# Performance work log

Hardware: AMD Instinct MI355X
Metric: run time of the kernel (lower is better)

Reference implementation:

```python
import jax, jax.numpy as jnp
import numpy as np

DMODEL = 1024
N_MAMBAS = 4
D_INNER = 2 * DMODEL          # expand = 2
D_STATE = 16                  # mamba_ssm default
D_CONV = 4                    # mamba_ssm default
DT_RANK = DMODEL // 16        # ceil(d_model/16) = 64


def setup_inputs() -> dict:
    key = jax.random.key(0)
    ks = jax.random.split(key, 8)
    B, L, n = 2, 4096, N_MAMBAS
    f32 = jnp.float32
    x = jax.random.normal(ks[0], (B, L, DMODEL), f32)
    in_w = jax.random.normal(ks[1], (n, 2 * D_INNER, DMODEL), f32) * 0.02
    conv_w = jax.random.normal(ks[2], (n, D_INNER, D_CONV), f32) * 0.1
    conv_b = jnp.zeros((n, D_INNER), f32)
    xproj_w = jax.random.normal(ks[3], (n, DT_RANK + 2 * D_STATE, D_INNER), f32) * 0.02
    dt_w = jax.random.normal(ks[4], (n, D_INNER, DT_RANK), f32) * 0.02
    # softplus-inverse of dt_init ~ 0.01 (mamba-style dt bias init)
    dt_b = jnp.log(jnp.expm1(jnp.full((n, D_INNER), 0.01, f32)))
    # S4D-real init: A_log = log(1..d_state)
    A_log = jnp.log(jnp.broadcast_to(jnp.arange(1, D_STATE + 1, dtype=f32), (n, D_INNER, D_STATE)))
    D_skip = jnp.ones((n, D_INNER), f32)
    out_w = jax.random.normal(ks[5], (n, DMODEL, D_INNER), f32) * 0.02
    return dict(x=x, in_w=in_w, conv_w=conv_w, conv_b=conv_b, xproj_w=xproj_w,
                dt_w=dt_w, dt_b=dt_b, A_log=A_log, D_skip=D_skip, out_w=out_w)


def _mamba(x, in_w, conv_w, conv_b, xproj_w, dt_w, dt_b, A_log, D_skip, out_w):
    # x: (B, Lc, D)
    Bb = x.shape[0]
    xz = jnp.einsum('bld,ed->ble', x, in_w)                 # (B, Lc, 2*D_INNER)
    xi, z = jnp.split(xz, 2, axis=-1)
    # causal depthwise conv over time
    xc = jnp.transpose(xi, (0, 2, 1))                       # (B, D_INNER, Lc)
    xc = jax.lax.conv_general_dilated(xc, conv_w[:, None, :], (1,),
                                      [(D_CONV - 1, 0)], feature_group_count=D_INNER)
    xi = jax.nn.silu(jnp.transpose(xc + conv_b[None, :, None], (0, 2, 1)))  # (B, Lc, D_INNER)
    proj = jnp.einsum('bld,ed->ble', xi, xproj_w)           # (B, Lc, DT_RANK + 2*D_STATE)
    dt = proj[..., :DT_RANK]
    Bm = proj[..., DT_RANK:DT_RANK + D_STATE]
    Cm = proj[..., DT_RANK + D_STATE:]
    dt = jax.nn.softplus(jnp.einsum('blr,dr->bld', dt, dt_w) + dt_b)  # (B, Lc, D_INNER)
    A = -jnp.exp(A_log)                                     # (D_INNER, D_STATE)

    def step(h, inp):
        dt_t, B_t, C_t, x_t = inp                           # (B,Di),(B,Ds),(B,Ds),(B,Di)
        dA = jnp.exp(dt_t[:, :, None] * A)                  # (B, Di, Ds)
        h = dA * h + dt_t[:, :, None] * B_t[:, None, :] * x_t[:, :, None]
        return h, jnp.einsum('bds,bs->bd', h, C_t)

    h0 = jnp.zeros((Bb, D_INNER, D_STATE), x.dtype)
    xs_t = (jnp.swapaxes(dt, 0, 1), jnp.swapaxes(Bm, 0, 1),
            jnp.swapaxes(Cm, 0, 1), jnp.swapaxes(xi, 0, 1))
    _, ys = jax.lax.scan(step, h0, xs_t)                    # (Lc, B, D_INNER)
    y = jnp.swapaxes(ys, 0, 1) + xi * D_skip                # (B, Lc, D_INNER)
    y = y * jax.nn.silu(z)
    return jnp.einsum('ble,de->bld', y, out_w)              # (B, Lc, D)


def reference(x, in_w, conv_w, conv_b, xproj_w, dt_w, dt_b, A_log, D_skip, out_w):
    B, L, D = x.shape
    n = N_MAMBAS
    # strided slices x[:, i::n] == reshape(B, L//n, n, D)[:, :, i]
    xs = jnp.transpose(x.reshape(B, L // n, n, D), (2, 0, 1, 3))   # (n, B, Lc, D)
    ys = jax.vmap(_mamba)(xs, in_w, conv_w, conv_b, xproj_w,
                          dt_w, dt_b, A_log, D_skip, out_w)        # (n, B, Lc, D)
    # torch.cat(dim=1) concatenates per-mamba outputs block-wise along seq
    return jnp.transpose(ys, (1, 0, 2, 3)).reshape(B, L, D)
```

## Files before the change

### kernel.cpp

```cpp
#include <hip/hip_runtime.h>
#include <math.h>

#define DM   1024
#define DI   2048
#define DSn  16
#define DTR  64
#define PW   96
#define LS   1024
#define NCH  16
#define CL   64
#define XKS  8

typedef unsigned short u16;
typedef unsigned int   u32;
typedef __attribute__((ext_vector_type(8))) short bf16x8;
typedef __attribute__((ext_vector_type(8))) unsigned short u16x8;
typedef __attribute__((ext_vector_type(4))) float f32x4;

__device__ __forceinline__ void split2(float f, u16& hi, u16& lo) {
  union { float f; unsigned int u; } v; v.f = f;
  hi = (u16)(v.u >> 16);
  union { unsigned int u; float f; } w; w.u = v.u & 0xffff0000u;
  union { float f; unsigned int u; } r; r.f = f - w.f;
  lo = (u16)(r.u >> 16);
}

template<int ROWS>
__device__ __forceinline__ bf16x8 frag(const u16* T, int l4, int row) {
  return *(const bf16x8*)&T[(l4 * ROWS + row) * 8];
}

template<int ROWS>
__device__ __forceinline__ void stage16f(const float* a, u16* Th, u16* Tl, int ra, int half) {
  #pragma unroll
  for (int q = 0; q < 2; ++q) {
    u16x8 vh, vl;
    #pragma unroll
    for (int c = 0; c < 8; ++c) {
      u16 h_, l_;
      split2(a[q * 8 + c], h_, l_);
      vh[c] = h_; vl[c] = l_;
    }
    const int slot = ((half * 2 + q) * ROWS + ra) * 8;
    *(u16x8*)&Th[slot] = vh;
    *(u16x8*)&Tl[slot] = vl;
  }
}

template<int ROWS>
__device__ __forceinline__ void stage8f(const float* a, u16* Th, u16* Tl, int rb, int kq) {
  u16x8 vh, vl;
  #pragma unroll
  for (int c = 0; c < 8; ++c) {
    u16 h_, l_;
    split2(a[c], h_, l_);
    vh[c] = h_; vl[c] = l_;
  }
  const int slot = (kq * ROWS + rb) * 8;
  *(u16x8*)&Th[slot] = vh;
  *(u16x8*)&Tl[slot] = vl;
}

__global__ __launch_bounds__(256) void k_split_x(
    const float* __restrict__ x, u16* __restrict__ xh, u16* __restrict__ xl, int ib0)
{
  const int idx = blockIdx.x * 256 + threadIdx.x;
  const int t = idx >> 8, kq = (idx & 255) * 4;
  const int gt = ib0 * 1024 + t;
  const int j = gt & (LS - 1), ib = gt >> 10;
  const int i = ib >> 1, bb = ib & 1;
  const float4 v = *(const float4*)&x[(size_t)(bb * 4096 + j * 4 + i) * DM + kq];
  ushort4 vh, vl;
  split2(v.x, vh.x, vl.x); split2(v.y, vh.y, vl.y);
  split2(v.z, vh.z, vl.z); split2(v.w, vh.w, vl.w);
  *(ushort4*)&xh[(size_t)t * DM + kq] = vh;
  *(ushort4*)&xl[(size_t)t * DM + kq] = vl;
}

#define KGP 2064
__global__ __launch_bounds__(512, 2) void k_inproj(
    const u16* __restrict__ xh, const u16* __restrict__ xl,
    const float* __restrict__ inwf,
    float* __restrict__ xz, int ib0, int swz)
{
  __shared__ __align__(16) u16 L[2][4][4][KGP];
  const int tid = threadIdx.x;
  int mblk, nblk;
  if (swz) {
    const int o = blockIdx.x;
    const int xcd = o & 7, within = o >> 3;
    mblk = xcd * 4 + (within & 3);
    nblk = within >> 2;
  } else {
    mblk = blockIdx.x; nblk = blockIdx.y;
  }
  const int m0 = mblk << 8, n0 = nblk << 8;
  const int ib = ib0 + (m0 >> 10);
  const int il = (ib >> 1) - (ib0 >> 1);
  const int ra = tid >> 1, half = tid & 1;
  const u16* Aph = xh + (size_t)(m0 + ra) * DM + half * 16;
  const u16* Apl = xl + (size_t)(m0 + ra) * DM + half * 16;
  const float* Bpf = inwf + ((size_t)il * 4096 + n0 + ra) * DM + half * 16;
  const int w = tid >> 6, lane = tid & 63;
  const int wr = w >> 2, wc = w & 3;
  const int l15 = lane & 15, l4 = lane >> 4;

  f32x4 acc[8][4];
  #pragma unroll
  for (int a_ = 0; a_ < 8; ++a_)
    #pragma unroll
    for (int b_ = 0; b_ < 4; ++b_) acc[a_][b_] = (f32x4)(0.f);

  u16x8 ah2[2], al2[2];
  float br[16];

  auto LOADG = [&](int kt) {
    const int k0 = kt * 32;
    ah2[0] = *(const u16x8*)(Aph + k0);
    ah2[1] = *(const u16x8*)(Aph + k0 + 8);
    al2[0] = *(const u16x8*)(Apl + k0);
    al2[1] = *(const u16x8*)(Apl + k0 + 8);
    *(f32x4*)&br[0]  = *(const f32x4*)(Bpf + k0);
    *(f32x4*)&br[4]  = *(const f32x4*)(Bpf + k0 + 4);
    *(f32x4*)&br[8]  = *(const f32x4*)(Bpf + k0 + 8);
    *(f32x4*)&br[12] = *(const f32x4*)(Bpf + k0 + 12);
  };
  auto STORE = [&](int b) {
    #pragma unroll
    for (int q = 0; q < 2; ++q) {
      const int kg = half * 2 + q;
      *(u16x8*)&L[b][0][kg][ra * 8] = ah2[q];
      *(u16x8*)&L[b][1][kg][ra * 8] = al2[q];
      u16x8 vh, vl;
      #pragma unroll
      for (int c = 0; c < 8; ++c) {
        u16 h_, l_;
        split2(br[q * 8 + c], h_, l_);
        vh[c] = h_; vl[c] = l_;
      }
      *(u16x8*)&L[b][2][kg][ra * 8] = vh;
      *(u16x8*)&L[b][3][kg][ra * 8] = vl;
    }
  };
  auto COMPUTE = [&](int b) {
    bf16x8 bh[4], bl[4];
    #pragma unroll
    for (int nf = 0; nf < 4; ++nf) {
      const int col = wc * 64 + nf * 16 + l15;
      bh[nf] = *(const bf16x8*)&L[b][2][l4][col * 8];
      bl[nf] = *(const bf16x8*)&L[b][3][l4][col * 8];
    }
    #pragma unroll
    for (int mf = 0; mf < 8; ++mf) {
      const int row = wr * 128 + mf * 16 + l15;
      bf16x8 ah = *(const bf16x8*)&L[b][0][l4][row * 8];
      bf16x8 al = *(const bf16x8*)&L[b][1][l4][row * 8];
      #pragma unroll
      for (int nf = 0; nf < 4; ++nf) {
        acc[mf][nf] = __builtin_amdgcn_mfma_f32_16x16x32_bf16(ah, bh[nf], acc[mf][nf], 0, 0, 0);
        acc[mf][nf] = __builtin_amdgcn_mfma_f32_16x16x32_bf16(ah, bl[nf], acc[mf][nf], 0, 0, 0);
        acc[mf][nf] = __builtin_amdgcn_mfma_f32_16x16x32_bf16(al, bh[nf], acc[mf][nf], 0, 0, 0);
      }
    }
  };

  const int nk = DM / 32;
  LOADG(0);
  STORE(0);
  if (nk > 1) LOADG(1);
  __syncthreads();
  for (int kt = 0; kt < nk; ++kt) {
    const int c = kt & 1;
    if (kt + 1 < nk) STORE(c ^ 1);
    if (kt + 2 < nk) LOADG(kt + 2);
    COMPUTE(c);
    __syncthreads();
  }

  #pragma unroll
  for (int mf = 0; mf < 8; ++mf) {
    const int row = m0 + wr * 128 + mf * 16 + l4 * 4;
    #pragma unroll
    for (int nf = 0; nf < 4; ++nf) {
      const int col = n0 + wc * 64 + nf * 16 + l15;
      #pragma unroll
      for (int r = 0; r < 4; ++r)
        xz[(size_t)(row + r) * (2 * DI) + col] = acc[mf][nf][r];
    }
  }
}

__global__ __launch_bounds__(256) void k_conv(
    const float* __restrict__ xz, const float* __restrict__ convw,
    const float* __restrict__ convb, float* __restrict__ xib,
    int ib0, int ntok)
{
  const int idx = blockIdx.x * 256 + threadIdx.x;
  if (idx >= ntok * (DI / 4)) return;
  const int t = idx / (DI / 4);
  const int c = (idx - t * (DI / 4)) * 4;
  const int j = t & (LS - 1);
  const int i = (ib0 + (t >> 10)) >> 1;
  float4 acc = *(const float4*)&convb[(size_t)i * DI + c];
  float4 wt[4];
  #pragma unroll
  for (int q = 0; q < 4; ++q)
    wt[q] = *(const float4*)&convw[((size_t)i * DI + c + q) * 4];
  #pragma unroll
  for (int k = 0; k < 4; ++k) {
    const int j2 = j + k - 3;
    if (j2 >= 0) {
      const float4 v = *(const float4*)&xz[(size_t)(t + k - 3) * (2 * DI) + c];
      acc.x = fmaf(v.x, ((const float*)&wt[0])[k], acc.x);
      acc.y = fmaf(v.y, ((const float*)&wt[1])[k], acc.y);
      acc.z = fmaf(v.z, ((const float*)&wt[2])[k], acc.z);
      acc.w = fmaf(v.w, ((const float*)&wt[3])[k], acc.w);
    }
  }
  float4 o;
  o.x = acc.x / (1.f + __expf(-acc.x));
  o.y = acc.y / (1.f + __expf(-acc.y));
  o.z = acc.z / (1.f + __expf(-acc.z));
  o.w = acc.w / (1.f + __expf(-acc.w));
  *(float4*)&xib[(size_t)t * DI + c] = o;
}

__global__ __launch_bounds__(256) void k_xproj_part(
    const float* __restrict__ xif, const float* __restrict__ xwf,
    float* __restrict__ Pp, int ib0, int ntok)
{
  __shared__ __align__(16) u16 Ah[4*64*8], Al[4*64*8];
  __shared__ __align__(16) u16 Bh[4*96*8], Bl[4*96*8];
  const int tid = threadIdx.x;
  const int m0 = blockIdx.x << 6;
  const int ks = blockIdx.y;
  const int kbase = ks * (DI / XKS);
  const int ib = ib0 + (m0 >> 10);
  const int il = (ib >> 1) - (ib0 >> 1);
  const int ra = tid >> 1, half = tid & 1;
  const bool hasA = (tid < 128);
  const bool hasB = (tid < 192);
  const float* Apf = xif + (size_t)(m0 + ra) * DI + kbase + half * 16;
  const float* Bpf = xwf + ((size_t)il * PW + ra) * DI + kbase + half * 16;
  const int w = tid >> 6, lane = tid & 63;
  const int l15 = lane & 15, l4 = lane >> 4;

  f32x4 acc[6];
  #pragma unroll
  for (int b_ = 0; b_ < 6; ++b_) acc[b_] = (f32x4)(0.f);

  float ar[16], br[16];
  if (hasA) {
    #pragma unroll
    for (int q = 0; q < 4; ++q) *(f32x4*)&ar[q*4] = *(const f32x4*)(Apf + q*4);
  }
  if (hasB) {
    #pragma unroll
    for (int q = 0; q < 4; ++q) *(f32x4*)&br[q*4] = *(const f32x4*)(Bpf + q*4);
  }
  const int nk = (DI / XKS) / 32;
  for (int kt = 0; kt < nk; ++kt) {
    __syncthreads();
    if (hasA) stage16f<64>(ar, Ah, Al, ra, half);
    if (hasB) stage16f<96>(br, Bh, Bl, ra, half);
    __syncthreads();
    if (kt + 1 < nk) {
      const int k0 = (kt + 1) * 32;
      if (hasA) {
        #pragma unroll
        for (int q = 0; q < 4; ++q) *(f32x4*)&ar[q*4] = *(const f32x4*)(Apf + k0 + q*4);
      }
      if (hasB) {
        #pragma unroll
        for (int q = 0; q < 4; ++q) *(f32x4*)&br[q*4] = *(const f32x4*)(Bpf + k0 + q*4);
      }
    }
    const int arow = w * 16 + l15;
    bf16x8 ah = frag<64>(Ah, l4, arow);
    bf16x8 al = frag<64>(Al, l4, arow);
    #pragma unroll
    for (int nf = 0; nf < 6; ++nf) {
      const int col = nf * 16 + l15;
      bf16x8 bh = frag<96>(Bh, l4, col);
      bf16x8 bl = frag<96>(Bl, l4, col);
      acc[nf] = __builtin_amdgcn_mfma_f32_16x16x32_bf16(ah, bh, acc[nf], 0, 0, 0);
      acc[nf] = __builtin_amdgcn_mfma_f32_16x16x32_bf16(ah, bl, acc[nf], 0, 0, 0);
      acc[nf] = __builtin_amdgcn_mfma_f32_16x16x32_bf16(al, bh, acc[nf], 0, 0, 0);
    }
  }
  float* outp = Pp + (size_t)ks * ntok * PW;
  const int row = m0 + w * 16 + l4 * 4;
  #pragma unroll
  for (int nf = 0; nf < 6; ++nf) {
    const int col = nf * 16 + l15;
    #pragma unroll
    for (int r = 0; r < 4; ++r)
      outp[(size_t)(row + r) * PW + col] = acc[nf][r];
  }
}

__global__ __launch_bounds__(256) void k_xproj_red(
    const float* __restrict__ Pp, float* __restrict__ projb, int ntok)
{
  const int idx = blockIdx.x * 256 + threadIdx.x;
  if (idx >= ntok * PW) return;
  const size_t plane = (size_t)ntok * PW;
  float s = 0.f;
  #pragma unroll
  for (int ks = 0; ks < XKS; ++ks) s += Pp[(size_t)ks * plane + idx];
  projb[idx] = s;
}

__global__ __launch_bounds__(256) void k_dtproj(
    const float* __restrict__ proj, const float* __restrict__ dtw,
    const float* __restrict__ dtbias, float* __restrict__ dtout,
    int dstride, int ib0)
{
  __shared__ float As[16][132];
  __shared__ float Bs[16][132];
  const int tid = threadIdx.x;
  const int n0 = blockIdx.x << 7;
  const int m0 = blockIdx.y << 7;
  const int ib = ib0 + (m0 >> 10);
  const int i  = ib >> 1;
  const int ar = tid >> 2, kq = tid & 3;
  const float* A0 = proj + (size_t)(m0 + ar) * PW + kq * 4;
  const float* A1 = A0 + (size_t)64 * PW;
  const float* Wb = dtw + (size_t)i * DI * DTR;
  const float* B0 = Wb + (size_t)(n0 + ar) * DTR + kq * 4;
  const float* B1 = B0 + (size_t)64 * DTR;
  const int tx = tid & 15, ty = tid >> 4;
  float acc[8][8] = {};
  for (int kt = 0; kt < DTR / 16; ++kt) {
    const int k0 = kt * 16;
    float4 a0 = *(const float4*)(A0 + k0);
    float4 a1 = *(const float4*)(A1 + k0);
    float4 b0 = *(const float4*)(B0 + k0);
    float4 b1 = *(const float4*)(B1 + k0);
    __syncthreads();
    As[kq*4+0][ar] = a0.x; As[kq*4+1][ar] = a0.y; As[kq*4+2][ar] = a0.z; As[kq*4+3][ar] = a0.w;
    As[kq*4+0][ar+64] = a1.x; As[kq*4+1][ar+64] = a1.y; As[kq*4+2][ar+64] = a1.z; As[kq*4+3][ar+64] = a1.w;
    Bs[kq*4+0][ar] = b0.x; Bs[kq*4+1][ar] = b0.y; Bs[kq*4+2][ar] = b0.z; Bs[kq*4+3][ar] = b0.w;
    Bs[kq*4+0][ar+64] = b1.x; Bs[kq*4+1][ar+64] = b1.y; Bs[kq*4+2][ar+64] = b1.z; Bs[kq*4+3][ar+64] = b1.w;
    __syncthreads();
    #pragma unroll
    for (int k = 0; k < 16; ++k) {
      const float4 av0 = *(const float4*)&As[k][ty*8];
      const float4 av1 = *(const float4*)&As[k][ty*8+4];
      const float4 bv0 = *(const float4*)&Bs[k][tx*8];
      const float4 bv1 = *(const float4*)&Bs[k][tx*8+4];
      const float aa[8] = {av0.x,av0.y,av0.z,av0.w,av1.x,av1.y,av1.z,av1.w};
      const float bv[8] = {bv0.x,bv0.y,bv0.z,bv0.w,bv1.x,bv1.y,bv1.z,bv1.w};
      #pragma unroll
      for (int r = 0; r < 8; ++r)
        #pragma unroll
        for (int c = 0; c < 8; ++c)
          acc[r][c] = fmaf(aa[r], bv[c], acc[r][c]);
    }
  }
  float bias[8];
  #pragma unroll
  for (int c = 0; c < 8; ++c) bias[c] = dtbias[(size_t)i * DI + n0 + tx*8 + c];
  #pragma unroll
  for (int r = 0; r < 8; ++r) {
    const int t = m0 + ty*8 + r;
    #pragma unroll
    for (int c = 0; c < 8; ++c) {
      float u = acc[r][c] + bias[c];
      float sp = (u > 20.f) ? u : log1pf(__expf(u));
      dtout[(size_t)t * dstride + n0 + tx*8 + c] = sp;
    }
  }
}

__global__ __launch_bounds__(256) void k_scan_part(
    const float* __restrict__ projb, const float* dtp, int dstride,
    const float* __restrict__ xib, const float* __restrict__ A_log,
    float* __restrict__ Pbuf, float* __restrict__ Hbuf, int ib0)
{
  const int d = blockIdx.x * 256 + threadIdx.x;
  const int ch = blockIdx.y, lib = blockIdx.z;
  const int i = (ib0 + lib) >> 1;
  const size_t gd = (size_t)i * DI + d;
  __shared__ float bs[CL][DSn];
  const size_t trow = (size_t)lib * LS + (size_t)ch * CL;
  for (int p = threadIdx.x; p < CL * DSn; p += 256) {
    const int jj = p >> 4, ss = p & 15;
    bs[jj][ss] = projb[(trow + jj) * PW + DTR + ss];
  }
  float A[DSn], P[DSn], h[DSn];
  #pragma unroll
  for (int s = 0; s < DSn; ++s) {
    A[s] = -__expf(A_log[gd * DSn + s]);
    P[s] = 1.f; h[s] = 0.f;
  }
  __syncthreads();
  float dt_c = dtp[trow * dstride + d];
  float xi_c = xib[trow * DI + d];
  for (int j = 0; j < CL; ++j) {
    float dt_n = 0.f, xi_n = 0.f;
    if (j + 1 < CL) {
      dt_n = dtp[(trow + j + 1) * dstride + d];
      xi_n = xib[(trow + j + 1) * DI + d];
    }
    const float dx = dt_c * xi_c;
    #pragma unroll
    for (int s = 0; s < DSn; ++s) {
      const float dA = __expf(dt_c * A[s]);
      P[s] *= dA;
      h[s] = fmaf(dA, h[s], dx * bs[j][s]);
    }
    dt_c = dt_n; xi_c = xi_n;
  }
  const size_t base = ((size_t)(lib * NCH + ch) * DSn) * DI + d;
  #pragma unroll
  for (int s = 0; s < DSn; ++s) {
    Pbuf[base + (size_t)s * DI] = P[s];
    Hbuf[base + (size_t)s * DI] = h[s];
  }
}

__global__ __launch_bounds__(256) void k_scan_mid(
    float* __restrict__ Pbuf, const float* __restrict__ Hbuf, int nib)
{
  const int idx = blockIdx.x * 256 + threadIdx.x;
  if (idx >= nib * DSn * DI) return;
  const int d = idx & (DI - 1);
  const int s = (idx >> 11) & 15;
  const int lib = idx >> 15;
  const size_t stride = (size_t)DSn * DI;
  const size_t base = ((size_t)lib * NCH * DSn + s) * DI + d;
  float carry = 0.f;
  for (int c = 0; c < NCH; ++c) {
    const size_t o = base + (size_t)c * stride;
    const float p = Pbuf[o];
    const float hl = Hbuf[o];
    Pbuf[o] = carry;
    carry = fmaf(p, carry, hl);
  }
}

__global__ __launch_bounds__(256) void k_scan_full(
    const float* __restrict__ projb, const float* dtp, int dstride,
    float* xibio, const float* xzz,
    const float* __restrict__ A_log, const float* __restrict__ D_skip,
    const float* __restrict__ Pbuf, int ib0)
{
  const int d = blockIdx.x * 256 + threadIdx.x;
  const int ch = blockIdx.y, lib = blockIdx.z;
  const int i = (ib0 + lib) >> 1;
  const size_t gd = (size_t)i * DI + d;
  __shared__ float bs[CL][2 * DSn];
  const size_t trow = (size_t)lib * LS + (size_t)ch * CL;
  for (int p = threadIdx.x; p < CL * 2 * DSn; p += 256) {
    const int jj = p >> 5, ss = p & 31;
    bs[jj][ss] = projb[(trow + jj) * PW + DTR + ss];
  }
  float A[DSn], h[DSn];
  const size_t hbase = ((size_t)(lib * NCH + ch) * DSn) * DI + d;
  #pragma unroll
  for (int s = 0; s < DSn; ++s) {
    A[s] = -__expf(A_log[gd * DSn + s]);
    h[s] = Pbuf[hbase + (size_t)s * DI];
  }
  const float Dsk = D_skip[gd];
  __syncthreads();
  float dt_c = dtp[trow * dstride + d];
  float xi_c = xibio[trow * DI + d];
  float z_c  = xzz[trow * (2 * DI) + DI + d];
  for (int j = 0; j < CL; ++j) {
    float dt_n = 0.f, xi_n = 0.f, z_n = 0.f;
    if (j + 1 < CL) {
      dt_n = dtp[(trow + j + 1) * dstride + d];
      xi_n = xibio[(trow + j + 1) * DI + d];
      z_n  = xzz[(trow + j + 1) * (2 * DI) + DI + d];
    }
    const float dx = dt_c * xi_c;
    float y = 0.f;
    #pragma unroll
    for (int s = 0; s < DSn; ++s) {
      const float dA = __expf(dt_c * A[s]);
      h[s] = fmaf(dA, h[s], dx * bs[j][s]);
      y = fmaf(h[s], bs[j][DSn + s], y);
    }
    const float sz = z_c / (1.f + __expf(-z_c));
    const float val = (y + xi_c * Dsk) * sz;
    u16 vh, vl;
    split2(val, vh, vl);
    ((u32*)xibio)[(trow + j) * DI + d] = ((u32)vh << 16) | (u32)vl;
    dt_c = dt_n; xi_c = xi_n; z_c = z_n;
  }
}

__global__ __launch_bounds__(256) void k_outproj(
    const u32* __restrict__ ybp, const float* __restrict__ owf,
    float* __restrict__ out, int ib0)
{
  __shared__ __align__(16) u16 Ah[4*128*8], Al[4*128*8];
  __shared__ __align__(16) u16 Bh[4*128*8], Bl[4*128*8];
  const int tid = threadIdx.x;
  const int m0 = blockIdx.x << 7;
  const int n0 = blockIdx.y << 7;
  const int ib = ib0 + (m0 >> 10);
  const int i = ib >> 1, bb = ib & 1;
  const int il = i - (ib0 >> 1);
  const int ra = tid >> 1, half = tid & 1;
  const u32* Ap = ybp + (size_t)(m0 + ra) * DI + half * 16;
  const int rb = tid >> 1;
  const float* Bpf = owf + ((size_t)il * DM + n0 + rb) * DI + half * 16;
  const int w = tid >> 6, lane = tid & 63;
  const int wr = w >> 1, wc = w & 1;
  const int l15 = lane & 15, l4 = lane >> 4;

  f32x4 acc[4][4];
  #pragma unroll
  for (int a_ = 0; a_ < 4; ++a_)
    #pragma unroll
    for (int b_ = 0; b_ < 4; ++b_) acc[a_][b_] = (f32x4)(0.f);

  uint4 qa[4];
  float br[16];
  qa[0] = *(const uint4*)(Ap);     qa[1] = *(const uint4*)(Ap + 4);
  qa[2] = *(const uint4*)(Ap + 8); qa[3] = *(const uint4*)(Ap + 12);
  #pragma unroll
  for (int q = 0; q < 4; ++q) *(f32x4*)&br[q*4] = *(const f32x4*)(Bpf + q*4);
  const int nk = DI / 32;
  for (int kt = 0; kt < nk; ++kt) {
    __syncthreads();
    #pragma unroll
    for (int g = 0; g < 2; ++g) {
      const u32 e[8] = { qa[2*g].x, qa[2*g].y, qa[2*g].z, qa[2*g].w,
                         qa[2*g+1].x, qa[2*g+1].y, qa[2*g+1].z, qa[2*g+1].w };
      u16x8 vh, vl;
      #pragma unroll
      for (int c = 0; c < 8; ++c) { vh[c] = (u16)(e[c] >> 16); vl[c] = (u16)(e[c] & 0xffffu); }
      const int slot = ((half*2+g)*128 + ra)*8;
      *(u16x8*)&Ah[slot] = vh;
      *(u16x8*)&Al[slot] = vl;
    }
    stage16f<128>(br, Bh, Bl, rb, half);
    __syncthreads();
    if (kt + 1 < nk) {
      const int k0 = (kt + 1) * 32;
      qa[0] = *(const uint4*)(Ap + k0);     qa[1] = *(const uint4*)(Ap + k0 + 4);
      qa[2] = *(const uint4*)(Ap + k0 + 8); qa[3] = *(const uint4*)(Ap + k0 + 12);
      #pragma unroll
      for (int q = 0; q < 4; ++q) *(f32x4*)&br[q*4] = *(const f32x4*)(Bpf + k0 + q*4);
    }
    bf16x8 ah[4], al[4];
    #pragma unroll
    for (int mf = 0; mf < 4; ++mf) {
      const int row = wr * 64 + mf * 16 + l15;
      ah[mf] = frag<128>(Ah, l4, row);
      al[mf] = frag<128>(Al, l4, row);
    }
    #pragma unroll
    for (int nf = 0; nf < 4; ++nf) {
      const int col = wc * 64 + nf * 16 + l15;
      bf16x8 bh = frag<128>(Bh, l4, col);
      bf16x8 bl = frag<128>(Bl, l4, col);
      #pragma unroll
      for (int mf = 0; mf < 4; ++mf) {
        acc[mf][nf] = __builtin_amdgcn_mfma_f32_16x16x32_bf16(ah[mf], bh, acc[mf][nf], 0, 0, 0);
        acc[mf][nf] = __builtin_amdgcn_mfma_f32_16x16x32_bf16(ah[mf], bl, acc[mf][nf], 0, 0, 0);
        acc[mf][nf] = __builtin_amdgcn_mfma_f32_16x16x32_bf16(al[mf], bh, acc[mf][nf], 0, 0, 0);
      }
    }
  }
  #pragma unroll
  for (int mf = 0; mf < 4; ++mf) {
    const int t0 = m0 + wr * 64 + mf * 16 + l4 * 4;
    #pragma unroll
    for (int nf = 0; nf < 4; ++nf) {
      const int col = n0 + wc * 64 + nf * 16 + l15;
      #pragma unroll
      for (int r = 0; r < 4; ++r) {
        const int j = (t0 + r) & (LS - 1);
        out[(size_t)(bb * 4096 + i * 1024 + j) * DM + col] = acc[mf][nf][r];
      }
    }
  }
}

extern "C" void kernel_launch(void* const* d_in, const int* in_sizes, int n_in,
                              void* d_out, int out_size, void* d_ws, size_t ws_size,
                              hipStream_t stream) {
  (void)in_sizes; (void)n_in; (void)out_size;
  const float* x       = (const float*)d_in[0];
  const float* in_w    = (const float*)d_in[1];
  const float* conv_w  = (const float*)d_in[2];
  const float* conv_b  = (const float*)d_in[3];
  const float* xproj_w = (const float*)d_in[4];
  const float* dt_w    = (const float*)d_in[5];
  const float* dt_b    = (const float*)d_in[6];
  const float* A_log   = (const float*)d_in[7];
  const float* D_skip  = (const float*)d_in[8];
  const float* out_w   = (const float*)d_in[9];
  float* out = (float*)d_out;
  const dim3 blk(256);

  const size_t needSP = ((size_t)8192 * 4096 + (size_t)8192 * 2048 + (size_t)8192 * 96) * 4;
  if (ws_size >= needSP) {
    const size_t nt = 8192;
    float* xz    = (float*)d_ws;
    float* xib   = xz + nt * (2 * DI);
    float* projb = xib + nt * DI;
    u16* xph  = (u16*)d_out;  u16* xpl  = xph + nt * DM;
    float* Pp = (float*)d_out;
    float* Pbuf = (float*)d_out;
    float* Hbuf = Pbuf + (size_t)8 * NCH * DSn * DI;
    float* dtz = xz;
    u32* ybp  = (u32*)xib;

    k_split_x<<<dim3((int)nt), blk, 0, stream>>>(x, xph, xpl, 0);
    k_inproj<<<dim3(512), dim3(512), 0, stream>>>(xph, xpl, in_w, xz, 0, 1);
    k_conv<<<dim3((int)(nt*(DI/4)/256)), blk, 0, stream>>>(xz, conv_w, conv_b, xib, 0, (int)nt);
    k_xproj_part<<<dim3((int)(nt/64), XKS), blk, 0, stream>>>(xib, xproj_w, Pp, 0, (int)nt);
    k_xproj_red<<<dim3((int)(nt*PW/256)), blk, 0, stream>>>(Pp, projb, (int)nt);
    k_dtproj<<<dim3(DI/128, (int)(nt/128)), blk, 0, stream>>>(projb, dt_w, dt_b, dtz, 2*DI, 0);
    k_scan_part<<<dim3(DI/256, NCH, 8), blk, 0, stream>>>(projb, dtz, 2*DI, xib, A_log, Pbuf, Hbuf, 0);
    k_scan_mid<<<dim3(8 * DSn * DI / 256), blk, 0, stream>>>(Pbuf, Hbuf, 8);
    k_scan_full<<<dim3(DI/256, NCH, 8), blk, 0, stream>>>(projb, dtz, 2*DI, xib, xz, A_log, D_skip, Pbuf, 0);
    k_outproj<<<dim3((int)(nt/128), 8), blk, 0, stream>>>(ybp, out_w, out, 0);
    return;
  }

  auto needFB = [](int nib) -> size_t { return (size_t)nib * 29753344ull; };
  const int step = (ws_size >= needFB(4)) ? 4 : 2;

  for (int ib0 = 0; ib0 < 8; ib0 += step) {
    const int nib = step;
    const size_t nt = (size_t)nib * LS;
    const int i0 = ib0 >> 1;
    float* xz    = (float*)d_ws;
    float* xib   = xz + nt * (2 * DI);
    float* projb = xib + nt * DI;
    float* SH    = projb + nt * PW;
    u16* xph  = (u16*)SH;  u16* xpl = xph + nt * DM;
    float* Pp = SH;
    float* Pbuf = SH;
    float* Hbuf = Pbuf + (size_t)nib * NCH * DSn * DI / 2;
    float* dtz = xz;
    u32* ybp  = (u32*)xib;

    k_split_x<<<dim3((int)nt), blk, 0, stream>>>(x, xph, xpl, ib0);
    k_inproj<<<dim3((int)(nt/256), 16), dim3(512), 0, stream>>>(xph, xpl, in_w + (size_t)i0*4096*DM, xz, ib0, 0);
    k_conv<<<dim3((int)(nt*(DI/4)/256)), blk, 0, stream>>>(xz, conv_w, conv_b, xib, ib0, (int)nt);
    k_xproj_part<<<dim3((int)(nt/64), XKS), blk, 0, stream>>>(xib, xproj_w + (size_t)i0*PW*DI, Pp, ib0, (int)nt);
    k_xproj_red<<<dim3((int)(nt*PW/256)), blk, 0, stream>>>(Pp, projb, (int)nt);
    k_dtproj<<<dim3(DI/128, (int)(nt/128)), blk, 0, stream>>>(projb, dt_w, dt_b, dtz, 2*DI, ib0);
    k_scan_part<<<dim3(DI/256, NCH, nib), blk, 0, stream>>>(projb, dtz, 2*DI, xib, A_log, Pbuf, Hbuf, ib0);
    k_scan_mid<<<dim3(nib * DSn * DI / 256), blk, 0, stream>>>(Pbuf, Hbuf, nib);
    k_scan_full<<<dim3(DI/256, NCH, nib), blk, 0, stream>>>(projb, dtz, 2*DI, xib, xz, A_log, D_skip, Pbuf, ib0);
    k_outproj<<<dim3((int)(nt/128), 8), blk, 0, stream>>>(ybp, out_w + (size_t)i0*DM*DI, out, ib0);
  }
}
```

Before: 627.9 us.

## Stream in_proj A tiles directly into LDS via global_load_lds

The in_proj GEMM now loads the pre-split bf16 hi/lo x tiles straight from global memory into LDS with global_load_lds DMA instead of passing them through registers. The LDS buffers are split into separate A and B arrays, and the k-loop is unrolled by two with static buffer indices. MFMA compute is wrapped in s_setprio raises. This is meant to cut VGPR pressure and VALU/LDS-store instructions in the staging path, but it relies on the DMA finishing before the barrier and on the layout matching the fragment reads.

After: 660.5 us. +5.2%, slower.

```diff
diff --git a/kernel.cpp b/kernel.cpp
--- a/kernel.cpp
+++ b/kernel.cpp
@@ -17,6 +17,10 @@
 typedef __attribute__((ext_vector_type(8))) unsigned short u16x8;
 typedef __attribute__((ext_vector_type(4))) float f32x4;
 
+#define GLOAD16(gp, lp) \
+  __builtin_amdgcn_global_load_lds((const __attribute__((address_space(1))) void*)(gp), \
+                                   (__attribute__((address_space(3))) void*)(lp), 16, 0, 0)
+
 __device__ __forceinline__ void split2(float f, u16& hi, u16& lo) {
   union { float f; unsigned int u; } v; v.f = f;
   hi = (u16)(v.u >> 16);
@@ -45,20 +49,6 @@
     *(u16x8*)&Th[slot] = vh;
     *(u16x8*)&Tl[slot] = vl;
   }
-}
-
-template<int ROWS>
-__device__ __forceinline__ void stage8f(const float* a, u16* Th, u16* Tl, int rb, int kq) {
-  u16x8 vh, vl;
-  #pragma unroll
-  for (int c = 0; c < 8; ++c) {
-    u16 h_, l_;
-    split2(a[c], h_, l_);
-    vh[c] = h_; vl[c] = l_;
-  }
-  const int slot = (kq * ROWS + rb) * 8;
-  *(u16x8*)&Th[slot] = vh;
-  *(u16x8*)&Tl[slot] = vl;
 }
 
 __global__ __launch_bounds__(256) void k_split_x(
@@ -83,7 +73,8 @@
     const float* __restrict__ inwf,
     float* __restrict__ xz, int ib0, int swz)
 {
-  __shared__ __align__(16) u16 L[2][4][4][KGP];
+  __shared__ __align__(16) u16 LA[2][2][4][KGP];
+  __shared__ __align__(16) u16 LB[2][2][4][KGP];
   const int tid = threadIdx.x;
   int mblk, nblk;
   if (swz) {
@@ -98,39 +89,45 @@
   const int ib = ib0 + (m0 >> 10);
   const int il = (ib >> 1) - (ib0 >> 1);
   const int ra = tid >> 1, half = tid & 1;
-  const u16* Aph = xh + (size_t)(m0 + ra) * DM + half * 16;
-  const u16* Apl = xl + (size_t)(m0 + ra) * DM + half * 16;
   const float* Bpf = inwf + ((size_t)il * 4096 + n0 + ra) * DM + half * 16;
   const int w = tid >> 6, lane = tid & 63;
   const int wr = w >> 2, wc = w & 3;
   const int l15 = lane & 15, l4 = lane >> 4;
 
+  const int c20 = w * 2, c21 = w * 2 + 1;
+  const int kg0 = c20 >> 2, rb0 = (c20 & 3) * 64;
+  const int kg1 = c21 >> 2, rb1 = (c21 & 3) * 64;
+  const u16* aH0 = xh + (size_t)(m0 + rb0 + lane) * DM + kg0 * 8;
+  const u16* aH1 = xh + (size_t)(m0 + rb1 + lane) * DM + kg1 * 8;
+  const u16* aL0 = xl + (size_t)(m0 + rb0 + lane) * DM + kg0 * 8;
+  const u16* aL1 = xl + (size_t)(m0 + rb1 + lane) * DM + kg1 * 8;
+
   f32x4 acc[8][4];
   #pragma unroll
   for (int a_ = 0; a_ < 8; ++a_)
     #pragma unroll
     for (int b_ = 0; b_ < 4; ++b_) acc[a_][b_] = (f32x4)(0.f);
 
-  u16x8 ah2[2], al2[2];
   float br[16];
 
-  auto LOADG = [&](int kt) {
+  auto LOADB = [&](int kt) {
     const int k0 = kt * 32;
-    ah2[0] = *(const u16x8*)(Aph + k0);
-    ah2[1] = *(const u16x8*)(Aph + k0 + 8);
-    al2[0] = *(const u16x8*)(Apl + k0);
-    al2[1] = *(const u16x8*)(Apl + k0 + 8);
     *(f32x4*)&br[0]  = *(const f32x4*)(Bpf + k0);
     *(f32x4*)&br[4]  = *(const f32x4*)(Bpf + k0 + 4);
     *(f32x4*)&br[8]  = *(const f32x4*)(Bpf + k0 + 8);
     *(f32x4*)&br[12] = *(const f32x4*)(Bpf + k0 + 12);
   };
-  auto STORE = [&](int b) {
+  auto DMAA = [&](int b, int kt) {
+    const int k0 = kt * 32;
+    GLOAD16(aH0 + k0, &LA[b][0][kg0][rb0 * 8]);
+    GLOAD16(aH1 + k0, &LA[b][0][kg1][rb1 * 8]);
+    GLOAD16(aL0 + k0, &LA[b][1][kg0][rb0 * 8]);
+    GLOAD16(aL1 + k0, &LA[b][1][kg1][rb1 * 8]);
+  };
+  auto STOREB = [&](int b) {
     #pragma unroll
     for (int q = 0; q < 2; ++q) {
       const int kg = half * 2 + q;
-      *(u16x8*)&L[b][0][kg][ra * 8] = ah2[q];
-      *(u16x8*)&L[b][1][kg][ra * 8] = al2[q];
       u16x8 vh, vl;
       #pragma unroll
       for (int c = 0; c < 8; ++c) {
@@ -138,8 +135,8 @@
         split2(br[q * 8 + c], h_, l_);
         vh[c] = h_; vl[c] = l_;
       }
-      *(u16x8*)&L[b][2][kg][ra * 8] = vh;
-      *(u16x8*)&L[b][3][kg][ra * 8] = vl;
+      *(u16x8*)&LB[b][0][kg][ra * 8] = vh;
+      *(u16x8*)&LB[b][1][kg][ra * 8] = vl;
     }
   };
   auto COMPUTE = [&](int b) {
@@ -147,14 +144,14 @@
     #pragma unroll
     for (int nf = 0; nf < 4; ++nf) {
       const int col = wc * 64 + nf * 16 + l15;
-      bh[nf] = *(const bf16x8*)&L[b][2][l4][col * 8];
-      bl[nf] = *(const bf16x8*)&L[b][3][l4][col * 8];
+      bh[nf] = *(const bf16x8*)&LB[b][0][l4][col * 8];
+      bl[nf] = *(const bf16x8*)&LB[b][1][l4][col * 8];
     }
     #pragma unroll
     for (int mf = 0; mf < 8; ++mf) {
       const int row = wr * 128 + mf * 16 + l15;
-      bf16x8 ah = *(const bf16x8*)&L[b][0][l4][row * 8];
-      bf16x8 al = *(const bf16x8*)&L[b][1][l4][row * 8];
+      bf16x8 ah = *(const bf16x8*)&LA[b][0][l4][row * 8];
+      bf16x8 al = *(const bf16x8*)&LA[b][1][l4][row * 8];
       #pragma unroll
       for (int nf = 0; nf < 4; ++nf) {
         acc[mf][nf] = __builtin_amdgcn_mfma_f32_16x16x32_bf16(ah, bh[nf], acc[mf][nf], 0, 0, 0);
@@ -165,16 +162,22 @@
   };
 
   const int nk = DM / 32;
-  LOADG(0);
-  STORE(0);
-  if (nk > 1) LOADG(1);
+  DMAA(0, 0);
+  LOADB(0);
+  STOREB(0);
+  LOADB(1);
   __syncthreads();
-  for (int kt = 0; kt < nk; ++kt) {
-    const int c = kt & 1;
-    if (kt + 1 < nk) STORE(c ^ 1);
-    if (kt + 2 < nk) LOADG(kt + 2);
+  auto STEP = [&](int kt, int c) {
+    if (kt + 1 < nk) { DMAA(c ^ 1, kt + 1); STOREB(c ^ 1); }
+    if (kt + 2 < nk) LOADB(kt + 2);
+    __builtin_amdgcn_s_setprio(1);
     COMPUTE(c);
+    __builtin_amdgcn_s_setprio(0);
     __syncthreads();
+  };
+  for (int kt = 0; kt < nk; kt += 2) {
+    STEP(kt, 0);
+    STEP(kt + 1, 1);
   }
 
   #pragma unroll
```
